# Optimization experiments

Hardware: AMD Instinct MI355X
Metric: run time of the kernel (lower is better)

The kernel has to match this reference:

```python
import jax, jax.numpy as jnp
import numpy as np

VTH = 1.0      # v_threshold
TAU = 2.0      # spikingjelly LIFNode default tau
ALPHA = 2.0    # ATan surrogate alpha
EPS = 1e-5     # BatchNorm eps
N_HEADS = 8
TOPK = 4       # routed regions per query region
REGION = 64    # tokens per region (4096 tokens -> 64 regions)


@jax.custom_vjp
def spike_fn(v):
    return (v >= VTH).astype(v.dtype)

def _spike_fwd(v):
    return (v >= VTH).astype(v.dtype), v

def _spike_bwd(v, g):
    sg = (ALPHA / 2.0) / (1.0 + (jnp.pi / 2.0 * ALPHA * (v - VTH)) ** 2)
    return (g * sg,)

spike_fn.defvjp(_spike_fwd, _spike_bwd)


def lif(x):
    # x: [T, B, L, D]; LIF with decay_input=True, hard reset to 0, detach_reset
    def step(v, xt):
        v = v + (xt - v) / TAU
        s = spike_fn(v)
        v = v * (1.0 - jax.lax.stop_gradient(s))
        return v, s
    _, s = jax.lax.scan(step, jnp.zeros_like(x[0]), x)
    return s


def batchnorm(x, gamma, beta):
    # torch BN1d over [T*B, D, L] in training mode == per-channel stats over (T,B,L)
    mean = x.mean(axis=(0, 1, 2))
    var = jnp.mean((x - mean) ** 2, axis=(0, 1, 2))
    return (x - mean) * jax.lax.rsqrt(var + EPS) * gamma + beta


def bilevel_attn(x, qkv_w, qkv_b, proj_w, proj_b):
    # x: [TB, L, D]
    TB, L, D = x.shape
    nreg = L // REGION
    hd = D // N_HEADS
    qkv = x @ qkv_w.T + qkv_b
    q, k, v = jnp.split(qkv, 3, axis=-1)
    qr = q.reshape(TB, nreg, REGION, D)
    kr = k.reshape(TB, nreg, REGION, D)
    vr = v.reshape(TB, nreg, REGION, D)
    # coarse region-level routing via mean-pooled q/k affinity
    aff = jnp.einsum('bnd,bmd->bnm', qr.mean(2), kr.mean(2))  # [TB, nreg, nreg]
    _, idx = jax.lax.top_k(aff, TOPK)                         # [TB, nreg, TOPK]
    gather = jax.vmap(lambda t, ix: t[ix])                    # per-sample region gather
    kg = gather(kr, idx).reshape(TB, nreg, TOPK * REGION, N_HEADS, hd)
    vg = gather(vr, idx).reshape(TB, nreg, TOPK * REGION, N_HEADS, hd)
    qh = qr.reshape(TB, nreg, REGION, N_HEADS, hd)
    logits = jnp.einsum('bnqhd,bnkhd->bnhqk', qh, kg) * (hd ** -0.5)
    p = jax.nn.softmax(logits, axis=-1)
    o = jnp.einsum('bnhqk,bnkhd->bnqhd', p, vg).reshape(TB, L, D)
    return o @ proj_w.T + proj_b


def setup_inputs() -> dict:
    key = jax.random.key(0)
    ks = jax.random.split(key, 8)
    T, B, Lt, L, D = 4, 2, 4, 1024, 256
    Ltot = Lt * L
    s = 0.02
    return {
        'x': jax.random.normal(ks[0], (T, B, Ltot, D), jnp.float32),
        'bn1_g': jnp.ones((D,), jnp.float32),
        'bn1_b': jnp.zeros((D,), jnp.float32),
        'bn2_g': jnp.ones((D,), jnp.float32),
        'bn2_b': jnp.zeros((D,), jnp.float32),
        'qkv_w': jax.random.normal(ks[1], (3 * D, D), jnp.float32) * s,
        'qkv_b': jnp.zeros((3 * D,), jnp.float32),
        'proj_w': jax.random.normal(ks[2], (D, D), jnp.float32) * s,
        'proj_b': jnp.zeros((D,), jnp.float32),
        'ffn_w1': jax.random.normal(ks[3], (4 * D, D), jnp.float32) * s,
        'ffn_b1': jnp.zeros((4 * D,), jnp.float32),
        'ffn_w2': jax.random.normal(ks[4], (D, 4 * D), jnp.float32) * s,
        'ffn_b2': jnp.zeros((D,), jnp.float32),
        'scale': jnp.ones((1,), jnp.float32) * 0.5,
        'Lt': Lt, 'b': B, 'L': L, 'dim': D,
    }


def reference(x, bn1_g, bn1_b, bn2_g, bn2_b, qkv_w, qkv_b, proj_w, proj_b,
              ffn_w1, ffn_b1, ffn_w2, ffn_b2, scale, Lt, b, L, dim):
    T = x.shape[0]
    Ltot = Lt * L
    # attention branch
    identity = x
    s1 = lif(batchnorm(x, bn1_g, bn1_b))
    a = bilevel_attn(s1.reshape(T * b, Ltot, dim), qkv_w, qkv_b, proj_w, proj_b)
    x = identity + a.reshape(T, b, Ltot, dim) * scale
    # ffn branch
    s2 = lif(batchnorm(x, bn2_g, bn2_b))
    h = jax.nn.gelu(s2 @ ffn_w1.T + ffn_b1, approximate=False) @ ffn_w2.T + ffn_b2
    return x + h * scale
```

## Files before the change

kernel.cpp:

```cpp
#include <hip/hip_runtime.h>
#include <hip/hip_bf16.h>
#include <math.h>

typedef __attribute__((ext_vector_type(8))) short short8;
typedef __attribute__((ext_vector_type(4))) float f32x4;

#define DIM 256
#define NROWS 32768
#define PERT 2097152
#define SAMP_TOK 4096

__device__ __forceinline__ float b2f(__hip_bfloat16 h){ return __bfloat162float(h); }
__device__ __forceinline__ __hip_bfloat16 f2b(float f){ return __float2bfloat16(f); }
__device__ __forceinline__ unsigned short f2bu(float f){
  __hip_bfloat16 h = __float2bfloat16(f);
  unsigned short u; __builtin_memcpy(&u, &h, 2); return u;
}

__device__ __forceinline__ void gl2lds16(const void* g, void* l){
  __builtin_amdgcn_global_load_lds(
      (const __attribute__((address_space(1))) unsigned int*)g,
      (__attribute__((address_space(3))) unsigned int*)l, 16, 0, 0);
}

__global__ void f2b_k(const float* __restrict__ in, __hip_bfloat16* __restrict__ out, int n){
  int i = blockIdx.x * 256 + threadIdx.x;
  if (i < n) out[i] = f2b(in[i]);
}

__global__ void bn_stats_k(const float* __restrict__ x, float* __restrict__ sum, float* __restrict__ sumsq){
  int c = threadIdx.x;
  size_t base = (size_t)blockIdx.x * 256 * DIM + c;
  float s = 0.f, s2 = 0.f;
  for (int i = 0; i < 256; ++i){
    float v = x[base + (size_t)i * DIM];
    s += v; s2 += v * v;
  }
  atomicAdd(&sum[c], s);
  atomicAdd(&sumsq[c], s2);
}

__global__ void bn_fin_k(const float* __restrict__ sum, const float* __restrict__ sumsq,
                         const float* __restrict__ g, const float* __restrict__ b,
                         float* __restrict__ a_out, float* __restrict__ b_out){
  int c = threadIdx.x;
  float mean = sum[c] * (1.f/32768.f);
  float var  = sumsq[c] * (1.f/32768.f) - mean*mean;
  float a = g[c] / sqrtf(var + 1e-5f);
  a_out[c] = a;
  b_out[c] = b[c] - mean * a;
}

__global__ void lif_k(const float* __restrict__ x, const float* __restrict__ av,
                      const float* __restrict__ bv, __hip_bfloat16* __restrict__ s){
  int e = blockIdx.x * blockDim.x + threadIdx.x;
  if (e >= PERT) return;
  int c = e & (DIM - 1);
  float a = av[c], b = bv[c];
  float v = 0.f;
  #pragma unroll
  for (int t = 0; t < 4; ++t){
    float xn = x[(size_t)t * PERT + e] * a + b;
    v += (xn - v) * 0.5f;
    float sp = (v >= 1.0f) ? 1.0f : 0.0f;
    s[(size_t)t * PERT + e] = f2b(sp);
    v = (v >= 1.0f) ? 0.f : v;
  }
}

__global__ void region_sum_k(const __hip_bfloat16* __restrict__ s, float* __restrict__ sm){
  int r = blockIdx.x, c = threadIdx.x;
  float acc = 0.f;
  size_t base = (size_t)r * 64 * DIM + c;
  for (int i = 0; i < 64; ++i) acc += b2f(s[base + (size_t)i * DIM]);
  sm[(size_t)r * DIM + c] = acc * 0.015625f;
}

__global__ void rgemm_k(const float* __restrict__ smr, const float* __restrict__ w,
                        const float* __restrict__ bias, float* __restrict__ qkm){
  __shared__ float arow[256];
  int r = blockIdx.x, t = threadIdx.x;
  arow[t] = smr[(size_t)r * 256 + t];
  __syncthreads();
  for (int j = t; j < 512; j += 256){
    const float* wr = w + (size_t)j * 256;
    float acc = 0.f;
    for (int k = 0; k < 256; ++k) acc += arow[k] * wr[k];
    qkm[(size_t)r * 512 + j] = acc + bias[j];
  }
}

template<int EPI>
__global__ __launch_bounds__(256) void gemm_bt(
    const __hip_bfloat16* __restrict__ A, const __hip_bfloat16* __restrict__ W,
    const float* __restrict__ bias, void* __restrict__ outp,
    const void* __restrict__ extra, const float* __restrict__ scaleptr,
    int K, int N)
{
  __shared__ __align__(16) short smem[8192];
  short* As = smem;
  short* Ws = smem + 4096;
  const int tid = threadIdx.x;
  const int bm = blockIdx.x, bn = blockIdx.y;
  const int lane = tid & 63;
  const int l16 = lane & 15, quad = lane >> 4;
  const int wv = tid >> 6;
  const int wm = (wv >> 1) << 6, wn = (wv & 1) << 6;

  const int sA0 = tid, sA1 = tid + 256;
  const int r0 = sA0 >> 2, c0 = ((sA0 & 3) - r0) & 3;
  const int r1 = sA1 >> 2, c1 = ((sA1 & 3) - r1) & 3;
  const __hip_bfloat16* gA0 = A + (size_t)(bm * 128 + r0) * K + c0 * 8;
  const __hip_bfloat16* gA1 = A + (size_t)(bm * 128 + r1) * K + c1 * 8;
  const __hip_bfloat16* gB0 = W + (size_t)(bn * 128 + r0) * K + c0 * 8;
  const __hip_bfloat16* gB1 = W + (size_t)(bn * 128 + r1) * K + c1 * 8;
  const int wslot = tid & ~63;
  short* ldsA0 = &As[(size_t)wslot * 8];
  short* ldsA1 = &As[(size_t)(wslot + 256) * 8];
  short* ldsB0 = &Ws[(size_t)wslot * 8];
  short* ldsB1 = &Ws[(size_t)(wslot + 256) * 8];

  int aoff[4], boff[4];
  #pragma unroll
  for (int i = 0; i < 4; ++i){
    int ar = wm + i * 16 + l16;
    aoff[i] = (ar * 4 + ((quad + ar) & 3)) * 8;
    int br = wn + i * 16 + l16;
    boff[i] = (br * 4 + ((quad + br) & 3)) * 8;
  }

  f32x4 zero = {0.f, 0.f, 0.f, 0.f};
  f32x4 acc[4][4];
  #pragma unroll
  for (int i = 0; i < 4; ++i)
    #pragma unroll
    for (int j = 0; j < 4; ++j) acc[i][j] = zero;

  for (int k0 = 0; k0 < K; k0 += 32){
    gl2lds16(gA0 + k0, ldsA0);
    gl2lds16(gA1 + k0, ldsA1);
    gl2lds16(gB0 + k0, ldsB0);
    gl2lds16(gB1 + k0, ldsB1);
    __syncthreads();
    short8 af[4];
    #pragma unroll
    for (int mi = 0; mi < 4; ++mi)
      af[mi] = *reinterpret_cast<const short8*>(&As[aoff[mi]]);
    #pragma unroll
    for (int ni = 0; ni < 4; ++ni){
      short8 bfr = *reinterpret_cast<const short8*>(&Ws[boff[ni]]);
      #pragma unroll
      for (int mi = 0; mi < 4; ++mi)
        acc[mi][ni] = __builtin_amdgcn_mfma_f32_16x16x32_bf16(af[mi], bfr, acc[mi][ni], 0, 0, 0);
    }
    __syncthreads();
  }

  if (EPI == 0 || EPI == 2){
    #pragma unroll
    for (int hh = 0; hh < 2; ++hh){
      if ((wv >> 1) == hh){
        #pragma unroll
        for (int ni = 0; ni < 4; ++ni){
          float bvl = bias[(bn << 7) + wn + ni * 16 + l16];
          #pragma unroll
          for (int mi = 0; mi < 4; ++mi){
            #pragma unroll
            for (int r = 0; r < 4; ++r){
              float v = acc[mi][ni][r] + bvl;
              if (EPI == 2) v = 0.5f * v * (1.0f + erff(v * 0.70710678118654752f));
              smem[(mi * 16 + (quad << 2) + r) * 128 + wn + ni * 16 + l16] = (short)f2bu(v);
            }
          }
        }
      }
      __syncthreads();
      #pragma unroll
      for (int i = 0; i < 4; ++i){
        int s = tid + i * 256;
        int row = s >> 4, cb = s & 15;
        short8 val = *reinterpret_cast<const short8*>(&smem[row * 128 + cb * 8]);
        *reinterpret_cast<short8*>((__hip_bfloat16*)outp +
            (size_t)((bm << 7) + (hh << 6) + row) * N + (bn << 7) + cb * 8) = val;
      }
      __syncthreads();
    }
  } else {
    const float sc = scaleptr[0];
    #pragma unroll
    for (int ni = 0; ni < 4; ++ni){
      int colg = (bn << 7) + wn + ni * 16 + l16;
      float bvl = bias[colg];
      #pragma unroll
      for (int mi = 0; mi < 4; ++mi){
        #pragma unroll
        for (int r = 0; r < 4; ++r){
          int rowg = (bm << 7) + wm + mi * 16 + (quad << 2) + r;
          float v = acc[mi][ni][r] + bvl;
          size_t off = (size_t)rowg * N + colg;
          ((float*)outp)[off] = ((const float*)extra)[off] + v * sc;
        }
      }
    }
  }
}

__global__ void topk_k(const float* __restrict__ qkm, int* __restrict__ idx){
  __shared__ float aff[64];
  int r = blockIdx.x;
  int m = threadIdx.x;
  int b = r >> 6;
  const float4* qrow = reinterpret_cast<const float4*>(qkm + (size_t)r * 512);
  const float4* krow = reinterpret_cast<const float4*>(qkm + (size_t)(b * 64 + m) * 512 + 256);
  float dot = 0.f;
  for (int d = 0; d < 64; ++d){
    float4 qv = qrow[d], kv = krow[d];
    dot += qv.x * kv.x + qv.y * kv.y + qv.z * kv.z + qv.w * kv.w;
  }
  aff[m] = dot;
  __syncthreads();
  if (m == 0){
    #pragma unroll
    for (int t = 0; t < 4; ++t){
      float best = -INFINITY; int bi = 0;
      for (int i = 0; i < 64; ++i){
        if (aff[i] > best){ best = aff[i]; bi = i; }
      }
      aff[bi] = -INFINITY;
      idx[r * 4 + t] = bi;
    }
  }
}

__global__ __launch_bounds__(256) void attn_mfma_k(
    const __hip_bfloat16* __restrict__ qkv, const int* __restrict__ idx,
    __hip_bfloat16* __restrict__ o_out, int rbase)
{
  __shared__ __align__(16) short lds[27136];
  __shared__ float den_s[4][16];
  const int rl = blockIdx.x;
  const int h  = blockIdx.y;
  const int rg = rbase + rl;
  const int bl = rl >> 6;
  const int tid = threadIdx.x;
  const int w = tid >> 6, lane = tid & 63;
  const int l16 = lane & 15, quad = lane >> 4;
  short* Pw = lds + 10240 + w * 4224;

  const int reg = idx[rg * 4 + (tid >> 6)] & 63;
  const size_t srow = (size_t)bl * SAMP_TOK + (size_t)reg * 64 + (tid & 63);
  const __hip_bfloat16* kvsrc = qkv + srow * 768 + 256 + (size_t)h * 32;

  const size_t qrow = (size_t)rl * 64 + w * 16 + l16;
  short8 qf = *reinterpret_cast<const short8*>(qkv + qrow * 768 + (size_t)h * 32 + quad * 8);

  uint4 vreg[4];
  #pragma unroll
  for (int c = 0; c < 4; ++c)
    vreg[c] = *reinterpret_cast<const uint4*>(kvsrc + 256 + c * 8);

  #pragma unroll
  for (int c = 0; c < 4; ++c)
    *reinterpret_cast<uint4*>(&lds[tid * 40 + c * 8]) =
      *reinterpret_cast<const uint4*>(kvsrc + c * 8);
  __syncthreads();

  f32x4 s[16];
  #pragma unroll
  for (int nt = 0; nt < 16; ++nt){
    short8 bf = *reinterpret_cast<const short8*>(&lds[(nt * 16 + l16) * 40 + quad * 8]);
    f32x4 z = {0.f, 0.f, 0.f, 0.f};
    s[nt] = __builtin_amdgcn_mfma_f32_16x16x32_bf16(qf, bf, z, 0, 0, 0);
  }
  __syncthreads();

  #pragma unroll
  for (int c = 0; c < 4; ++c){
    short8 vv = *reinterpret_cast<short8*>(&vreg[c]);
    #pragma unroll
    for (int e = 0; e < 8; ++e)
      lds[(c * 8 + e) * 264 + tid] = vv[e];
  }

  float m4[4] = {-1e30f, -1e30f, -1e30f, -1e30f};
  #pragma unroll
  for (int nt = 0; nt < 16; ++nt)
    #pragma unroll
    for (int r = 0; r < 4; ++r) m4[r] = fmaxf(m4[r], s[nt][r]);
  #pragma unroll
  for (int xm = 1; xm < 16; xm <<= 1)
    #pragma unroll
    for (int r = 0; r < 4; ++r) m4[r] = fmaxf(m4[r], __shfl_xor(m4[r], xm));
  float d4[4] = {0.f, 0.f, 0.f, 0.f};
  #pragma unroll
  for (int nt = 0; nt < 16; ++nt)
    #pragma unroll
    for (int r = 0; r < 4; ++r){
      float e = __expf((s[nt][r] - m4[r]) * 0.17677669529663687f);
      s[nt][r] = e; d4[r] += e;
    }
  #pragma unroll
  for (int xm = 1; xm < 16; xm <<= 1)
    #pragma unroll
    for (int r = 0; r < 4; ++r) d4[r] += __shfl_xor(d4[r], xm);
  if (l16 == 0){
    #pragma unroll
    for (int r = 0; r < 4; ++r) den_s[w][quad * 4 + r] = d4[r];
  }
  #pragma unroll
  for (int nt = 0; nt < 16; ++nt)
    #pragma unroll
    for (int r = 0; r < 4; ++r)
      Pw[(quad * 4 + r) * 264 + nt * 16 + l16] = (short)f2bu(s[nt][r]);
  __syncthreads();

  f32x4 o0 = {0.f, 0.f, 0.f, 0.f}, o1 = o0;
  #pragma unroll
  for (int kk = 0; kk < 8; ++kk){
    short8 pb = *reinterpret_cast<const short8*>(&Pw[l16 * 264 + kk * 32 + quad * 8]);
    short8 a0 = *reinterpret_cast<const short8*>(&lds[l16 * 264 + kk * 32 + quad * 8]);
    short8 a1 = *reinterpret_cast<const short8*>(&lds[(16 + l16) * 264 + kk * 32 + quad * 8]);
    o0 = __builtin_amdgcn_mfma_f32_16x16x32_bf16(a0, pb, o0, 0, 0, 0);
    o1 = __builtin_amdgcn_mfma_f32_16x16x32_bf16(a1, pb, o1, 0, 0, 0);
  }
  float inv = 1.f / den_s[w][l16];
  size_t obase = ((size_t)rl * 64 + w * 16 + l16) * 256 + (size_t)h * 32;
  unsigned pk0 = (unsigned)f2bu(o0[0] * inv) | ((unsigned)f2bu(o0[1] * inv) << 16);
  unsigned pk1 = (unsigned)f2bu(o0[2] * inv) | ((unsigned)f2bu(o0[3] * inv) << 16);
  unsigned pk2 = (unsigned)f2bu(o1[0] * inv) | ((unsigned)f2bu(o1[1] * inv) << 16);
  unsigned pk3 = (unsigned)f2bu(o1[2] * inv) | ((unsigned)f2bu(o1[3] * inv) << 16);
  *reinterpret_cast<uint2*>(o_out + obase + quad * 4)      = make_uint2(pk0, pk1);
  *reinterpret_cast<uint2*>(o_out + obase + 16 + quad * 4) = make_uint2(pk2, pk3);
}

extern "C" void kernel_launch(void* const* d_in, const int* in_sizes, int n_in,
                              void* d_out, int out_size, void* d_ws, size_t ws_size,
                              hipStream_t stream)
{
  const float* x      = (const float*)d_in[0];
  const float* bn1_g  = (const float*)d_in[1];
  const float* bn1_b  = (const float*)d_in[2];
  const float* bn2_g  = (const float*)d_in[3];
  const float* bn2_b  = (const float*)d_in[4];
  const float* qkv_w  = (const float*)d_in[5];
  const float* qkv_b  = (const float*)d_in[6];
  const float* proj_w = (const float*)d_in[7];
  const float* proj_b = (const float*)d_in[8];
  const float* ffn_w1 = (const float*)d_in[9];
  const float* ffn_b1 = (const float*)d_in[10];
  const float* ffn_w2 = (const float*)d_in[11];
  const float* ffn_b2 = (const float*)d_in[12];
  const float* scale  = (const float*)d_in[13];
  float* x2 = (float*)d_out;

  char* ws = (char*)d_ws;
  const size_t MB = 1024 * 1024;
  float* sum1 = (float*)(ws + 0);
  float* sq1  = (float*)(ws + 1024);
  float* sum2 = (float*)(ws + 2048);
  float* sq2  = (float*)(ws + 3072);
  float* a1   = (float*)(ws + 4096);
  float* b1   = (float*)(ws + 5120);
  float* a2   = (float*)(ws + 6144);
  float* b2   = (float*)(ws + 7168);
  int*   idxb = (int*)(ws + 8192);
  float* smr  = (float*)(ws + 16384);
  float* qkm  = (float*)(ws + 540672);
  __hip_bfloat16* qkv_wb  = (__hip_bfloat16*)(ws + 1589248);
  __hip_bfloat16* proj_wb = (__hip_bfloat16*)(ws + 1982464);
  __hip_bfloat16* ffn_w1b = (__hip_bfloat16*)(ws + 2113536);
  __hip_bfloat16* ffn_w2b = (__hip_bfloat16*)(ws + 2637824);
  __hip_bfloat16* s1 = (__hip_bfloat16*)(ws + 4 * MB);
  __hip_bfloat16* s2 = s1;
  char* chunkbuf = ws + 20 * MB;

  size_t avail = (ws_size > 20 * MB) ? (ws_size - 20 * MB) : (8 * MB);
  int nc = (avail >= 64 * MB) ? 8 : (avail >= 32 * MB) ? 4 : (avail >= 16 * MB) ? 2 : 1;
  int crows = 32768;
  while ((size_t)crows * 2048 > avail && crows > 2048) crows >>= 1;

  __hip_bfloat16* qkvc = (__hip_bfloat16*)chunkbuf;
  __hip_bfloat16* oc   = (__hip_bfloat16*)(chunkbuf + (size_t)nc * 6 * MB);
  __hip_bfloat16* h1   = (__hip_bfloat16*)chunkbuf;

  hipMemsetAsync(d_ws, 0, 4096, stream);

  f2b_k<<<(196608 + 255) / 256, 256, 0, stream>>>(qkv_w, qkv_wb, 196608);
  f2b_k<<<(65536 + 255) / 256, 256, 0, stream>>>(proj_w, proj_wb, 65536);
  f2b_k<<<(262144 + 255) / 256, 256, 0, stream>>>(ffn_w1, ffn_w1b, 262144);
  f2b_k<<<(262144 + 255) / 256, 256, 0, stream>>>(ffn_w2, ffn_w2b, 262144);

  bn_stats_k<<<128, 256, 0, stream>>>(x, sum1, sq1);
  bn_fin_k<<<1, 256, 0, stream>>>(sum1, sq1, bn1_g, bn1_b, a1, b1);
  lif_k<<<PERT / 256, 256, 0, stream>>>(x, a1, b1, s1);
  region_sum_k<<<512, 256, 0, stream>>>(s1, smr);
  rgemm_k<<<512, 256, 0, stream>>>(smr, qkv_w, qkv_b, qkm);
  topk_k<<<512, 64, 0, stream>>>(qkm, idxb);

  const int nchunkA = 8 / nc;
  for (int c = 0; c < nchunkA; ++c){
    const size_t ro = (size_t)c * nc * SAMP_TOK;
    gemm_bt<0><<<dim3(nc * SAMP_TOK / 128, 6), 256, 0, stream>>>(
        s1 + ro * 256, qkv_wb, qkv_b, qkvc, nullptr, nullptr, 256, 768);
    attn_mfma_k<<<dim3(nc * 64, 8), 256, 0, stream>>>(qkvc, idxb, oc, c * nc * 64);
    gemm_bt<1><<<dim3(nc * SAMP_TOK / 128, 2), 256, 0, stream>>>(
        oc, proj_wb, proj_b, x2 + ro * 256, x + ro * 256, scale, 256, 256);
  }

  bn_stats_k<<<128, 256, 0, stream>>>(x2, sum2, sq2);
  bn_fin_k<<<1, 256, 0, stream>>>(sum2, sq2, bn2_g, bn2_b, a2, b2);
  lif_k<<<PERT / 256, 256, 0, stream>>>(x2, a2, b2, s2);
  const int nchunkF = 32768 / crows;
  for (int c = 0; c < nchunkF; ++c){
    const size_t ro = (size_t)c * crows;
    gemm_bt<2><<<dim3(crows / 128, 8), 256, 0, stream>>>(
        s2 + ro * 256, ffn_w1b, ffn_b1, h1, nullptr, nullptr, 256, 1024);
    gemm_bt<3><<<dim3(crows / 128, 2), 256, 0, stream>>>(
        h1, ffn_w2b, ffn_b2, x2 + ro * 256, x2 + ro * 256, scale, 1024, 256);
  }
}
```

Before: 398.0 us.

## Load GEMM MFMA fragments directly from global into registers with double buffering

Replaces the LDS-staged GEMM (global_load_lds plus barriers each K step) with per-wave direct global loads of MFMA fragments into registers, double-buffered across 32-wide K halves. K becomes a template parameter so the loop fully unrolls. This removes LDS traffic and the two barriers per K iteration. In exchange, each wave reloads its A and W tiles from global/L2 with no sharing between waves, which doubles global load traffic, and the strided 16-byte row loads coalesce less well than before.

```diff
diff --git a/kernel.cpp b/kernel.cpp
--- a/kernel.cpp
+++ b/kernel.cpp
@@ -15,12 +15,6 @@
 __device__ __forceinline__ unsigned short f2bu(float f){
   __hip_bfloat16 h = __float2bfloat16(f);
   unsigned short u; __builtin_memcpy(&u, &h, 2); return u;
-}
-
-__device__ __forceinline__ void gl2lds16(const void* g, void* l){
-  __builtin_amdgcn_global_load_lds(
-      (const __attribute__((address_space(1))) unsigned int*)g,
-      (__attribute__((address_space(3))) unsigned int*)l, 16, 0, 0);
 }
 
 __global__ void f2b_k(const float* __restrict__ in, __hip_bfloat16* __restrict__ out, int n){
@@ -90,16 +84,13 @@
   }
 }
 
-template<int EPI>
-__global__ __launch_bounds__(256) void gemm_bt(
+template<int EPI, int K>
+__global__ __launch_bounds__(256) void gemm_rt(
     const __hip_bfloat16* __restrict__ A, const __hip_bfloat16* __restrict__ W,
     const float* __restrict__ bias, void* __restrict__ outp,
-    const void* __restrict__ extra, const float* __restrict__ scaleptr,
-    int K, int N)
+    const void* __restrict__ extra, const float* __restrict__ scaleptr, int N)
 {
-  __shared__ __align__(16) short smem[8192];
-  short* As = smem;
-  short* Ws = smem + 4096;
+  __shared__ __align__(16) short cs[8192];
   const int tid = threadIdx.x;
   const int bm = blockIdx.x, bn = blockIdx.y;
   const int lane = tid & 63;
@@ -107,53 +98,45 @@
   const int wv = tid >> 6;
   const int wm = (wv >> 1) << 6, wn = (wv & 1) << 6;
 
-  const int sA0 = tid, sA1 = tid + 256;
-  const int r0 = sA0 >> 2, c0 = ((sA0 & 3) - r0) & 3;
-  const int r1 = sA1 >> 2, c1 = ((sA1 & 3) - r1) & 3;
-  const __hip_bfloat16* gA0 = A + (size_t)(bm * 128 + r0) * K + c0 * 8;
-  const __hip_bfloat16* gA1 = A + (size_t)(bm * 128 + r1) * K + c1 * 8;
-  const __hip_bfloat16* gB0 = W + (size_t)(bn * 128 + r0) * K + c0 * 8;
-  const __hip_bfloat16* gB1 = W + (size_t)(bn * 128 + r1) * K + c1 * 8;
-  const int wslot = tid & ~63;
-  short* ldsA0 = &As[(size_t)wslot * 8];
-  short* ldsA1 = &As[(size_t)(wslot + 256) * 8];
-  short* ldsB0 = &Ws[(size_t)wslot * 8];
-  short* ldsB1 = &Ws[(size_t)(wslot + 256) * 8];
-
-  int aoff[4], boff[4];
+  const __hip_bfloat16* Ab = A + (size_t)(bm * 128 + wm + l16) * K + quad * 8;
+  const __hip_bfloat16* Wb = W + (size_t)(bn * 128 + wn + l16) * K + quad * 8;
+
+  f32x4 acc[4][4];
+  #pragma unroll
+  for (int i = 0; i < 4; ++i)
+    #pragma unroll
+    for (int j = 0; j < 4; ++j) acc[i][j] = (f32x4){0.f, 0.f, 0.f, 0.f};
+
+  short8 a0[4], b0[4], a1[4], b1[4];
   #pragma unroll
   for (int i = 0; i < 4; ++i){
-    int ar = wm + i * 16 + l16;
-    aoff[i] = (ar * 4 + ((quad + ar) & 3)) * 8;
-    int br = wn + i * 16 + l16;
-    boff[i] = (br * 4 + ((quad + br) & 3)) * 8;
-  }
-
-  f32x4 zero = {0.f, 0.f, 0.f, 0.f};
-  f32x4 acc[4][4];
-  #pragma unroll
-  for (int i = 0; i < 4; ++i)
-    #pragma unroll
-    for (int j = 0; j < 4; ++j) acc[i][j] = zero;
-
-  for (int k0 = 0; k0 < K; k0 += 32){
-    gl2lds16(gA0 + k0, ldsA0);
-    gl2lds16(gA1 + k0, ldsA1);
-    gl2lds16(gB0 + k0, ldsB0);
-    gl2lds16(gB1 + k0, ldsB1);
-    __syncthreads();
-    short8 af[4];
-    #pragma unroll
-    for (int mi = 0; mi < 4; ++mi)
-      af[mi] = *reinterpret_cast<const short8*>(&As[aoff[mi]]);
-    #pragma unroll
-    for (int ni = 0; ni < 4; ++ni){
-      short8 bfr = *reinterpret_cast<const short8*>(&Ws[boff[ni]]);
+    a0[i] = *reinterpret_cast<const short8*>(Ab + (size_t)i * 16 * K);
+    b0[i] = *reinterpret_cast<const short8*>(Wb + (size_t)i * 16 * K);
+  }
+  #pragma unroll
+  for (int k0 = 0; k0 < K; k0 += 64){
+    #pragma unroll
+    for (int i = 0; i < 4; ++i){
+      a1[i] = *reinterpret_cast<const short8*>(Ab + (size_t)i * 16 * K + k0 + 32);
+      b1[i] = *reinterpret_cast<const short8*>(Wb + (size_t)i * 16 * K + k0 + 32);
+    }
+    #pragma unroll
+    for (int ni = 0; ni < 4; ++ni)
       #pragma unroll
       for (int mi = 0; mi < 4; ++mi)
-        acc[mi][ni] = __builtin_amdgcn_mfma_f32_16x16x32_bf16(af[mi], bfr, acc[mi][ni], 0, 0, 0);
-    }
-    __syncthreads();
+        acc[mi][ni] = __builtin_amdgcn_mfma_f32_16x16x32_bf16(a0[mi], b0[ni], acc[mi][ni], 0, 0, 0);
+    if (k0 + 64 < K){
+      #pragma unroll
+      for (int i = 0; i < 4; ++i){
+        a0[i] = *reinterpret_cast<const short8*>(Ab + (size_t)i * 16 * K + k0 + 64);
+        b0[i] = *reinterpret_cast<const short8*>(Wb + (size_t)i * 16 * K + k0 + 64);
+      }
+    }
+    #pragma unroll
+    for (int ni = 0; ni < 4; ++ni)
+      #pragma unroll
+      for (int mi = 0; mi < 4; ++mi)
+        acc[mi][ni] = __builtin_amdgcn_mfma_f32_16x16x32_bf16(a1[mi], b1[ni], acc[mi][ni], 0, 0, 0);
   }
 
   if (EPI == 0 || EPI == 2){
@@ -169,7 +152,7 @@
             for (int r = 0; r < 4; ++r){
               float v = acc[mi][ni][r] + bvl;
               if (EPI == 2) v = 0.5f * v * (1.0f + erff(v * 0.70710678118654752f));
-              smem[(mi * 16 + (quad << 2) + r) * 128 + wn + ni * 16 + l16] = (short)f2bu(v);
+              cs[(mi * 16 + (quad << 2) + r) * 128 + wn + ni * 16 + l16] = (short)f2bu(v);
             }
           }
         }
@@ -179,7 +162,7 @@
       for (int i = 0; i < 4; ++i){
         int s = tid + i * 256;
         int row = s >> 4, cb = s & 15;
-        short8 val = *reinterpret_cast<const short8*>(&smem[row * 128 + cb * 8]);
+        short8 val = *reinterpret_cast<const short8*>(&cs[row * 128 + cb * 8]);
         *reinterpret_cast<short8*>((__hip_bfloat16*)outp +
             (size_t)((bm << 7) + (hh << 6) + row) * N + (bn << 7) + cb * 8) = val;
       }
@@ -400,11 +383,11 @@
   const int nchunkA = 8 / nc;
   for (int c = 0; c < nchunkA; ++c){
     const size_t ro = (size_t)c * nc * SAMP_TOK;
-    gemm_bt<0><<<dim3(nc * SAMP_TOK / 128, 6), 256, 0, stream>>>(
-        s1 + ro * 256, qkv_wb, qkv_b, qkvc, nullptr, nullptr, 256, 768);
+    gemm_rt<0, 256><<<dim3(nc * SAMP_TOK / 128, 6), 256, 0, stream>>>(
+        s1 + ro * 256, qkv_wb, qkv_b, qkvc, nullptr, nullptr, 768);
     attn_mfma_k<<<dim3(nc * 64, 8), 256, 0, stream>>>(qkvc, idxb, oc, c * nc * 64);
-    gemm_bt<1><<<dim3(nc * SAMP_TOK / 128, 2), 256, 0, stream>>>(
-        oc, proj_wb, proj_b, x2 + ro * 256, x + ro * 256, scale, 256, 256);
+    gemm_rt<1, 256><<<dim3(nc * SAMP_TOK / 128, 2), 256, 0, stream>>>(
+        oc, proj_wb, proj_b, x2 + ro * 256, x + ro * 256, scale, 256);
   }
 
   bn_stats_k<<<128, 256, 0, stream>>>(x2, sum2, sq2);
@@ -413,9 +396,9 @@
   const int nchunkF = 32768 / crows;
   for (int c = 0; c < nchunkF; ++c){
     const size_t ro = (size_t)c * crows;
-    gemm_bt<2><<<dim3(crows / 128, 8), 256, 0, stream>>>(
-        s2 + ro * 256, ffn_w1b, ffn_b1, h1, nullptr, nullptr, 256, 1024);
-    gemm_bt<3><<<dim3(crows / 128, 2), 256, 0, stream>>>(
-        h1, ffn_w2b, ffn_b2, x2 + ro * 256, x2 + ro * 256, scale, 1024, 256);
-  }
-}
+    gemm_rt<2, 256><<<dim3(crows / 128, 8), 256, 0, stream>>>(
+        s2 + ro * 256, ffn_w1b, ffn_b1, h1, nullptr, nullptr, 1024);
+    gemm_rt<3, 1024><<<dim3(crows / 128, 2), 256, 0, stream>>>(
+        h1, ffn_w2b, ffn_b2, x2 + ro * 256, x2 + ro * 256, scale, 256);
+  }
+}
```

Result: slower. 566.0 us (+42.2%).
